# Kernel tuning notes

Hardware: AMD Instinct MI355X
Metric: run time of the kernel (lower is better)

Reference implementation:

```python
import jax, jax.numpy as jnp
import numpy as np

T, B, V = 50, 128, 8000          # seq_len, batch, inputDimSize
A = 728                          # numAncestors
NEMB = V + A                     # rows of W_emb
E, H, ATT, C, L = 128, 128, 100, 283, 5


def setup_inputs() -> dict:
    key = jax.random.key(0)
    ks = jax.random.split(key, 12)
    x = jax.random.normal(ks[0], (T, B, V), jnp.float32)
    mask = jnp.ones((T, B), jnp.float32)
    leaves = jax.random.randint(ks[1], (V, L), 0, NEMB)
    ancestors = jax.random.randint(ks[2], (V, L), 0, NEMB)
    W_emb = jax.random.uniform(ks[3], (NEMB, E), jnp.float32)
    W_attention = jax.random.uniform(ks[4], (2 * E, ATT), jnp.float32)
    b_attention = jnp.zeros((ATT,), jnp.float32)
    v_attention = jax.random.uniform(ks[5], (ATT,), jnp.float32)
    gru_w_ih = jax.random.normal(ks[6], (3 * H, E), jnp.float32) * 0.1
    gru_w_hh = jax.random.normal(ks[7], (3 * H, H), jnp.float32) * 0.1
    gru_b_ih = jnp.zeros((3 * H,), jnp.float32)
    gru_b_hh = jnp.zeros((3 * H,), jnp.float32)
    W_output = jax.random.uniform(ks[8], (H, C), jnp.float32) * 0.1
    b_output = jnp.zeros((C,), jnp.float32)
    return {"x": x, "mask": mask, "W_emb": W_emb,
            "W_attention": W_attention, "b_attention": b_attention,
            "v_attention": v_attention, "gru_w_ih": gru_w_ih,
            "gru_w_hh": gru_w_hh, "gru_b_ih": gru_b_ih,
            "gru_b_hh": gru_b_hh, "W_output": W_output,
            "b_output": b_output, "leaves": leaves, "ancestors": ancestors}


def reference(x, mask, W_emb, W_attention, b_attention, v_attention,
              gru_w_ih, gru_w_hh, gru_b_ih, gru_b_hh,
              W_output, b_output, leaves, ancestors):
    # --- Attention over ontology ancestors (gather + MLP + softmax + reduce) ---
    le = W_emb[leaves]       # [V, L, E]
    an = W_emb[ancestors]    # [V, L, E]
    att_in = jnp.concatenate([le, an], axis=-1)              # [V, L, 2E]
    mlp = jnp.tanh(att_in @ W_attention + b_attention)       # [V, L, ATT]
    pre = mlp @ v_attention                                  # [V, L]
    att = jax.nn.softmax(pre, axis=1)                        # softmax over ancestors
    emb = jnp.einsum('vle,vl->ve', an, att)                  # [V, E]

    # --- project multi-hot visits into embedding space ---
    x_emb = jnp.tanh(jnp.einsum('tbv,ve->tbe', x, emb))      # [T, B, E]

    # --- torch-style single-layer GRU via scan (time-major) ---
    def cell(h, xt):
        gx = xt @ gru_w_ih.T + gru_b_ih                      # [B, 3H]
        gh = h @ gru_w_hh.T + gru_b_hh
        xr, xz, xn = jnp.split(gx, 3, axis=-1)
        hr, hz, hn = jnp.split(gh, 3, axis=-1)
        r = jax.nn.sigmoid(xr + hr)
        z = jax.nn.sigmoid(xz + hz)
        n = jnp.tanh(xn + r * hn)
        h_new = (1.0 - z) * n + z * h
        return h_new, h_new

    h0 = jnp.zeros((B, H), x_emb.dtype)
    _, hidden = jax.lax.scan(cell, h0, x_emb)                # [T, B, H]

    # dropout_rate = 0 -> identity
    # exp / sum == softmax over the class dim
    out = jax.nn.softmax(hidden @ W_output + b_output, axis=2)  # [T, B, C]
    return out * mask[:, :, None]
```

## Files before the change

### kernel.cpp

```cpp
#include <hip/hip_runtime.h>


typedef unsigned short u16;
typedef unsigned int   u32;
typedef short bf16x8 __attribute__((ext_vector_type(8)));
typedef float f32x4  __attribute__((ext_vector_type(4)));

typedef __attribute__((address_space(1))) u32 gas_u32;
typedef __attribute__((address_space(3))) u32 las_u32;

union U4 { u32 u[4]; bf16x8 v; uint4 q; };

__device__ __forceinline__ float uaf(u32 u){ union{u32 u; float f;} c; c.u=u; return c.f; }
__device__ __forceinline__ u32 fau(float f){ union{u32 u; float f;} c; c.f=f; return c.u; }
__device__ __forceinline__ u16 f2bf(float f){ u32 u=fau(f); return (u16)((u + 0x7fffu + ((u>>16)&1u))>>16); }
__device__ __forceinline__ float sigm(float x){ return 1.f/(1.f+__expf(-x)); }

__device__ __forceinline__ void gll16(const void* g, void* l){
    __builtin_amdgcn_global_load_lds((const gas_u32*)g, (las_u32*)l, 16, 0, 0);
}

__device__ __forceinline__ void split8(const float* f, bf16x8* hi, bf16x8* lo){
    U4 H, L;
    #pragma unroll
    for (int j=0;j<4;++j){
        float f0=f[2*j], f1=f[2*j+1];
        u32 u0=fau(f0), u1=fau(f1);
        u32 t0=u0+0x7fffu+((u0>>16)&1u);
        u32 t1=u1+0x7fffu+((u1>>16)&1u);
        u32 h1=t1&0xffff0000u;
        H.u[j]=(t0>>16)|h1;
        float l0=f0-uaf(t0&0xffff0000u);
        float l1=f1-uaf(h1);
        u32 v0=fau(l0), v1=fau(l1);
        u32 s0=v0+0x7fffu+((v0>>16)&1u);
        u32 s1=v1+0x7fffu+((v1>>16)&1u);
        L.u[j]=(s0>>16)|(s1&0xffff0000u);
    }
    *hi=H.v; *lo=L.v;
}

__device__ __forceinline__ void split1(float f, u16& h, u16& l){
    u32 u=fau(f); u32 t=u+0x7fffu+((u>>16)&1u); h=(u16)(t>>16);
    float lf=f-uaf(t&0xffff0000u); l=f2bf(lf);
}

#define MFMA(a,b,c) __builtin_amdgcn_mfma_f32_16x16x32_bf16(a,b,c,0,0,0)

__global__ __launch_bounds__(256,1) void prep_watt_kernel(
    const float* __restrict__ W_att, u16* __restrict__ WT_h, u16* __restrict__ WT_l)
{
    int n=blockIdx.x, k=threadIdx.x;
    float f = (n<100)? W_att[k*100+n] : 0.f;
    u16 h,l; split1(f,h,l);
    WT_h[n*256+k]=h; WT_l[n*256+k]=l;
}

__global__ __launch_bounds__(256,1) void prep_whh_kernel(
    const float* __restrict__ whh, u32* __restrict__ out)
{
    int i=blockIdx.x*256+threadIdx.x;
    int j=i>>6, p=i&63;
    u32 a=(u32)f2bf(whh[j*128+2*p]);
    u32 b=(u32)f2bf(whh[j*128+2*p+1]);
    out[i]=a|(b<<16);
}

__global__ __launch_bounds__(256,1) void transpose_wih_kernel(
    const float* __restrict__ w_ih, float* __restrict__ w_ihT)
{
    int i=blockIdx.x*256+threadIdx.x;
    int e=i/384, j=i-e*384;
    w_ihT[i]=w_ih[j*128+e];
}

__global__ __launch_bounds__(256,1) void attn_mlp_kernel(
    const float* __restrict__ W_emb, const float* __restrict__ b_att,
    const float* __restrict__ v_att, const int* __restrict__ leaves,
    const int* __restrict__ anc, const u16* __restrict__ WT_h,
    const u16* __restrict__ WT_l, float* __restrict__ emb_f)
{
    __shared__ __align__(16) char smem[61440];
    short* Ah=(short*)smem;
    short* Al=(short*)(smem+16384);
    short* Bh=(short*)(smem+32768);
    short* Bl=(short*)(smem+47104);
    float* mlp_s=(float*)smem;
    __shared__ float s_pre[128];
    __shared__ float s_vatt[112];
    __shared__ float s_attw[128];
    __shared__ int   s_leaf[128], s_anc[128];

    const int tid=threadIdx.x;
    const int wave=tid>>6, lane=tid&63;
    const int vb5=blockIdx.x*125;

    if (tid<125){ s_leaf[tid]=leaves[vb5+tid]; s_anc[tid]=anc[vb5+tid]; }
    else if (tid<128){ s_leaf[tid]=leaves[vb5]; s_anc[tid]=anc[vb5]; }
    if (tid<100) s_vatt[tid]=v_att[tid];

    f32x4 acc[2][7];
    const f32x4 zf={0.f,0.f,0.f,0.f};
    #pragma unroll
    for (int mi=0;mi<2;++mi)
        #pragma unroll
        for (int ni=0;ni<7;++ni) acc[mi][ni]=zf;

    const int fr=lane&15, fq=lane>>4;

    for (int kc=0;kc<4;++kc){
        __syncthreads();
        {
            int r=tid>>1, seg=tid&1;
            int src=(kc<2)? s_leaf[r] : s_anc[r];
            const float* srcp = W_emb + (size_t)src*128 + (kc&1)*64 + seg*32;
            float buf[32];
            #pragma unroll
            for (int i=0;i<8;++i) *(f32x4*)(buf+4*i) = *(const f32x4*)(srcp+4*i);
            #pragma unroll
            for (int j=0;j<4;++j){
                bf16x8 hv, lv; split8(buf+8*j, &hv, &lv);
                U4 H,L; H.v=hv; L.v=lv;
                *(uint4*)&Ah[r*64+seg*32+j*8] = H.q;
                *(uint4*)&Al[r*64+seg*32+j*8] = L.q;
            }
        }
        for (int c=wave;c<14;c+=4){
            size_t go=(size_t)(c*8+(lane>>3))*512 + (size_t)kc*128 + (size_t)(lane&7)*16;
            gll16((const char*)WT_h+go, Bh+c*512);
            gll16((const char*)WT_l+go, Bl+c*512);
        }
        __syncthreads();

        #pragma unroll
        for (int ks=0;ks<2;++ks){
            bf16x8 ah[2],al[2],bh[7],bl[7];
            #pragma unroll
            for (int mi=0;mi<2;++mi){
                int row=wave*32+mi*16+fr;
                ah[mi]=*(const bf16x8*)&Ah[row*64+ks*32+fq*8];
                al[mi]=*(const bf16x8*)&Al[row*64+ks*32+fq*8];
            }
            #pragma unroll
            for (int ni=0;ni<7;++ni){
                int rowb=ni*16+fr;
                bh[ni]=*(const bf16x8*)&Bh[rowb*64+ks*32+fq*8];
                bl[ni]=*(const bf16x8*)&Bl[rowb*64+ks*32+fq*8];
            }
            #pragma unroll
            for (int mi=0;mi<2;++mi)
                #pragma unroll
                for (int ni=0;ni<7;++ni){
                    acc[mi][ni]=MFMA(ah[mi],bh[ni],acc[mi][ni]);
                    acc[mi][ni]=MFMA(ah[mi],bl[ni],acc[mi][ni]);
                    acc[mi][ni]=MFMA(al[mi],bh[ni],acc[mi][ni]);
                }
        }
    }
    __syncthreads();
    #pragma unroll
    for (int ni=0;ni<7;++ni){
        int col=ni*16+fr;
        float bb=(col<100)? b_att[col] : 0.f;
        #pragma unroll
        for (int mi=0;mi<2;++mi){
            int rb=wave*32+mi*16+fq*4;
            #pragma unroll
            for (int r=0;r<4;++r)
                mlp_s[(rb+r)*112+col]=tanhf(acc[mi][ni][r]+bb);
        }
    }
    __syncthreads();
    if (tid<128){
        float s=0.f;
        for (int n=0;n<100;++n) s+=mlp_s[tid*112+n]*s_vatt[n];
        s_pre[tid]=s;
    }
    __syncthreads();
    if (tid<25){
        float p[5], mx=-1e30f;
        #pragma unroll
        for (int l=0;l<5;++l){ p[l]=s_pre[tid*5+l]; mx=fmaxf(mx,p[l]); }
        float s=0.f;
        #pragma unroll
        for (int l=0;l<5;++l){ p[l]=__expf(p[l]-mx); s+=p[l]; }
        float inv=1.f/s;
        #pragma unroll
        for (int l=0;l<5;++l) s_attw[tid*5+l]=p[l]*inv;
    }
    __syncthreads();
    for (int o=tid;o<3200;o+=256){
        int v=o>>7, e=o&127;
        float s=0.f;
        #pragma unroll
        for (int l=0;l<5;++l)
            s += s_attw[v*5+l]*W_emb[(size_t)s_anc[v*5+l]*128+e];
        emb_f[(size_t)(blockIdx.x*25+v)*128+e]=s;
    }
}

__global__ __launch_bounds__(256,1) void emb_split_kernel(
    const float* __restrict__ emb_f, u16* __restrict__ hiT, u16* __restrict__ loT)
{
    __shared__ float tile[64*128];
    const int tid=threadIdx.x;
    const int vb=blockIdx.x*64;
    for (int i=tid;i<2048;i+=256){
        int row=i>>5, q=i&31;
        *(f32x4*)&tile[row*128+q*4] = *(const f32x4*)&emb_f[(size_t)(vb+row)*128+q*4];
    }
    __syncthreads();
    u32* hw=(u32*)hiT; u32* lw=(u32*)loT;
    for (int o=tid;o<4096;o+=256){
        int e=o>>5, p=o&31;
        float f0=tile[(2*p)*128+e], f1=tile[(2*p+1)*128+e];
        u16 h0,l0,h1,l1; split1(f0,h0,l0); split1(f1,h1,l1);
        size_t base=(size_t)e*4000 + (size_t)(vb>>1) + p;
        hw[base]=(u32)h0|((u32)h1<<16);
        lw[base]=(u32)l0|((u32)l1<<16);
    }
}

__global__ __launch_bounds__(256,1) void gemm_xemb_kernel(
    const float* __restrict__ x, const u16* __restrict__ bhT, const u16* __restrict__ blT,
    float* __restrict__ partials)
{
    __shared__ __align__(16) float Asf[128*64];
    __shared__ __align__(16) short Bh[128*64];
    __shared__ __align__(16) short Bl[128*64];

    const int tid=threadIdx.x, wave=tid>>6, lane=tid&63;
    const int mt=blockIdx.x%50, ks=blockIdx.x/50;
    const int mbase=mt*128;
    const int k0=ks*1600;

    f32x4 acc[4][4];
    const f32x4 zf={0.f,0.f,0.f,0.f};
    #pragma unroll
    for (int i=0;i<4;++i)
        #pragma unroll
        for (int j=0;j<4;++j) acc[i][j]=zf;

    const char* xb=(const char*)x;
    const char* bhb=(const char*)bhT;
    const char* blb=(const char*)blT;
    const int mrow=(wave>>1)*64, ncol=(wave&1)*64;
    const int fr=lane&15, fq=lane>>4;

    for (int kk=k0; kk<k0+1600; kk+=64){
        __syncthreads();
        #pragma unroll
        for (int cc=0;cc<8;++cc){
            int c=wave*8+cc;
            int row=c*4+(lane>>4);
            gll16(xb + (size_t)(mbase+row)*32000 + (size_t)kk*4 + (size_t)(lane&15)*16,
                  &Asf[c*256]);
        }
        #pragma unroll
        for (int cc=0;cc<4;++cc){
            int c=wave*4+cc;
            int row=c*8+(lane>>3);
            size_t go=(size_t)row*16000 + (size_t)kk*2 + (size_t)(lane&7)*16;
            gll16(bhb+go, &Bh[c*512]);
            gll16(blb+go, &Bl[c*512]);
        }
        __syncthreads();

        #pragma unroll
        for (int kh=0;kh<2;++kh){
            bf16x8 ah[4],al[4],bh[4],bl[4];
            #pragma unroll
            for (int i=0;i<4;++i)
                split8(&Asf[(mrow+i*16+fr)*64 + kh*32 + fq*8], &ah[i], &al[i]);
            #pragma unroll
            for (int j=0;j<4;++j){
                bh[j]=*(const bf16x8*)&Bh[(ncol+j*16+fr)*64+kh*32+fq*8];
                bl[j]=*(const bf16x8*)&Bl[(ncol+j*16+fr)*64+kh*32+fq*8];
            }
            #pragma unroll
            for (int i=0;i<4;++i)
                #pragma unroll
                for (int j=0;j<4;++j){
                    acc[i][j]=MFMA(ah[i],bh[j],acc[i][j]);
                    acc[i][j]=MFMA(ah[i],bl[j],acc[i][j]);
                    acc[i][j]=MFMA(al[i],bh[j],acc[i][j]);
                }
        }
    }

    float* pout=partials + ((size_t)ks*6400+mbase)*128;
    #pragma unroll
    for (int i=0;i<4;++i)
        #pragma unroll
        for (int j=0;j<4;++j)
            #pragma unroll
            for (int r=0;r<4;++r)
                pout[(size_t)(mrow+i*16+fq*4+r)*128 + ncol+j*16+fr]=acc[i][j][r];
}

__global__ __launch_bounds__(256,1) void sum_tanh_kernel(
    const float* __restrict__ partials, float* __restrict__ x_emb)
{
    int i=blockIdx.x*256+threadIdx.x;
    float s=0.f;
    #pragma unroll
    for (int k=0;k<5;++k) s+=partials[(size_t)k*819200+i];
    x_emb[i]=tanhf(s);
}

__global__ __launch_bounds__(128,1) void gx_gemm_kernel(
    const float* __restrict__ x_emb, const float* __restrict__ w_ihT,
    const float* __restrict__ b_ih, float* __restrict__ GX)
{
    __shared__ float sx[2048];
    const int tid=threadIdx.x;
    const int rb=blockIdx.x*16;
    for (int i=tid;i<2048;i+=128) sx[i]=x_emb[(size_t)rb*128+i];
    __syncthreads();

    float acc0[16],acc1[16],acc2[16];
    #pragma unroll
    for (int r=0;r<16;++r){ acc0[r]=0.f; acc1[r]=0.f; acc2[r]=0.f; }
    for (int e=0;e<128;++e){
        float w0=w_ihT[e*384+tid];
        float w1=w_ihT[e*384+tid+128];
        float w2=w_ihT[e*384+tid+256];
        #pragma unroll
        for (int r=0;r<16;++r){
            float xv=sx[r*128+e];
            acc0[r]=fmaf(xv,w0,acc0[r]);
            acc1[r]=fmaf(xv,w1,acc1[r]);
            acc2[r]=fmaf(xv,w2,acc2[r]);
        }
    }
    float b0=b_ih[tid], b1=b_ih[tid+128], b2=b_ih[tid+256];
    #pragma unroll
    for (int r=0;r<16;++r){
        float* gp=GX+(size_t)(rb+r)*384;
        gp[tid]=acc0[r]+b0;
        gp[tid+128]=acc1[r]+b1;
        gp[tid+256]=acc2[r]+b2;
    }
}

__global__ __launch_bounds__(384,1) void gru_scan_kernel(
    const u32* __restrict__ whh_p, const float* __restrict__ b_hh,
    const float* __restrict__ GX, float* __restrict__ hidden)
{
    __shared__ __align__(16) float sh[128];
    __shared__ float sgh[384];
    __shared__ float sgx[384];
    const int tid=threadIdx.x, b=blockIdx.x;

    u32 wreg[64];
    #pragma unroll
    for (int p=0;p<64;++p) wreg[p]=whh_p[tid*64+p];
    if (tid<128) sh[tid]=0.f;
    const float bb=b_hh[tid];
    __syncthreads();

    const f32x4* sh4=(const f32x4*)sh;
    for (int t=0;t<50;++t){
        float acc=0.f;
        #pragma unroll
        for (int q=0;q<32;++q){
            f32x4 h4=sh4[q];
            u32 a=wreg[2*q], c=wreg[2*q+1];
            acc=fmaf(uaf(a<<16),        h4.x,acc);
            acc=fmaf(uaf(a&0xffff0000u),h4.y,acc);
            acc=fmaf(uaf(c<<16),        h4.z,acc);
            acc=fmaf(uaf(c&0xffff0000u),h4.w,acc);
        }
        sgh[tid]=acc+bb;
        sgx[tid]=GX[((size_t)t*128+b)*384+tid];
        __syncthreads();
        if (tid<128){
            float r=sigm(sgx[tid]+sgh[tid]);
            float z=sigm(sgx[128+tid]+sgh[128+tid]);
            float n=tanhf(sgx[256+tid]+r*sgh[256+tid]);
            float hn=(1.f-z)*n+z*sh[tid];
            hidden[((size_t)t*128+b)*128+tid]=hn;
            sh[tid]=hn;
        }
        __syncthreads();
    }
}

__global__ __launch_bounds__(128,1) void logits_kernel(
    const float* __restrict__ hidden, const float* __restrict__ W_out,
    const float* __restrict__ b_out, float* __restrict__ logits)
{
    __shared__ float shd[2048];
    const int tid=threadIdx.x;
    const int rb=blockIdx.x*16;
    for (int i=tid;i<2048;i+=128) shd[i]=hidden[(size_t)rb*128+i];
    __syncthreads();

    const int c0=tid, c1=tid+128, c2=tid+256;
    const bool v2=(c2<283);
    float acc0[16],acc1[16],acc2[16];
    #pragma unroll
    for (int r=0;r<16;++r){ acc0[r]=0.f; acc1[r]=0.f; acc2[r]=0.f; }
    for (int h=0;h<128;++h){
        const float* wr=W_out+h*283;
        float w0=wr[c0];
        float w1=wr[c1];
        float w2=v2? wr[c2] : 0.f;
        #pragma unroll
        for (int r=0;r<16;++r){
            float hv=shd[r*128+h];
            acc0[r]=fmaf(hv,w0,acc0[r]);
            acc1[r]=fmaf(hv,w1,acc1[r]);
            acc2[r]=fmaf(hv,w2,acc2[r]);
        }
    }
    float b0=b_out[c0], b1=b_out[c1], b2v=v2? b_out[c2] : 0.f;
    #pragma unroll
    for (int r=0;r<16;++r){
        float* lp=logits+(size_t)(rb+r)*283;
        lp[c0]=acc0[r]+b0;
        lp[c1]=acc1[r]+b1;
        if (v2) lp[c2]=acc2[r]+b2v;
    }
}

__global__ __launch_bounds__(256,1) void softmax_mask_kernel(
    const float* __restrict__ logits, const float* __restrict__ mask,
    float* __restrict__ out)
{
    const int wave=threadIdx.x>>6, lane=threadIdx.x&63;
    const int m=blockIdx.x*4+wave;
    const float* lp=logits+(size_t)m*283;
    float v[5];
    float mx=-1e30f;
    #pragma unroll
    for (int i=0;i<5;++i){
        int c=lane+i*64;
        v[i]=(c<283)? lp[c] : -1e30f;
        mx=fmaxf(mx,v[i]);
    }
    #pragma unroll
    for (int off=32;off>0;off>>=1) mx=fmaxf(mx,__shfl_xor(mx,off,64));
    float s=0.f;
    #pragma unroll
    for (int i=0;i<5;++i){
        int c=lane+i*64;
        v[i]=(c<283)? __expf(v[i]-mx) : 0.f;
        s+=v[i];
    }
    #pragma unroll
    for (int off=32;off>0;off>>=1) s+=__shfl_xor(s,off,64);
    const float sc=mask[m]/s;
    float* op=out+(size_t)m*283;
    #pragma unroll
    for (int i=0;i<5;++i){
        int c=lane+i*64;
        if (c<283) op[c]=v[i]*sc;
    }
}

extern "C" void kernel_launch(void* const* d_in, const int* in_sizes, int n_in,
                              void* d_out, int out_size, void* d_ws, size_t ws_size,
                              hipStream_t stream) {
    const float* x      = (const float*)d_in[0];
    const float* mask   = (const float*)d_in[1];
    const float* W_emb  = (const float*)d_in[2];
    const float* W_att  = (const float*)d_in[3];
    const float* b_att  = (const float*)d_in[4];
    const float* v_att  = (const float*)d_in[5];
    const float* w_ih   = (const float*)d_in[6];
    const float* w_hh   = (const float*)d_in[7];
    const float* b_ih   = (const float*)d_in[8];
    const float* b_hh   = (const float*)d_in[9];
    const float* W_out  = (const float*)d_in[10];
    const float* b_out  = (const float*)d_in[11];
    const int* leaves   = (const int*)d_in[12];
    const int* anc      = (const int*)d_in[13];
    float* out = (float*)d_out;

    char* w = (char*)d_ws;
    u16*   WT_h    = (u16*)(w + 0);
    u16*   WT_l    = (u16*)(w + 57344);
    u32*   whh_p   = (u32*)(w + 114688);
    float* w_ihT   = (float*)(w + 212992);
    u16*   emb_hiT = (u16*)(w + 409600);
    u16*   emb_loT = (u16*)(w + 2457600);
    float* x_emb   = (float*)(w + 4505600);
    float* hidden  = (float*)(w + 7782400);
    float* emb_f   = (float*)(w + 11059200);
    float* partials= (float*)(w + 11059200);
    float* GX      = (float*)(w + 11059200);
    float* logits  = (float*)(w + 11059200);

    prep_watt_kernel<<<112, 256, 0, stream>>>(W_att, WT_h, WT_l);
    prep_whh_kernel<<<96, 256, 0, stream>>>(w_hh, whh_p);
    transpose_wih_kernel<<<192, 256, 0, stream>>>(w_ih, w_ihT);
    attn_mlp_kernel<<<320, 256, 0, stream>>>(W_emb, b_att, v_att, leaves, anc,
                                             WT_h, WT_l, emb_f);
    emb_split_kernel<<<125, 256, 0, stream>>>(emb_f, emb_hiT, emb_loT);
    gemm_xemb_kernel<<<250, 256, 0, stream>>>(x, emb_hiT, emb_loT, partials);
    sum_tanh_kernel<<<3200, 256, 0, stream>>>(partials, x_emb);
    gx_gemm_kernel<<<400, 128, 0, stream>>>(x_emb, w_ihT, b_ih, GX);
    gru_scan_kernel<<<128, 384, 0, stream>>>(whh_p, b_hh, GX, hidden);
    logits_kernel<<<400, 128, 0, stream>>>(hidden, W_out, b_out, logits);
    softmax_mask_kernel<<<1600, 256, 0, stream>>>(logits, mask, out);
}
```

Measured before the change: 549.8 us.

## Shrink x_emb GEMM tiles with swizzled LDS and bf16 hidden state in GRU scan

The x·emb GEMM moves from 128x128 tiles over 250 blocks to 32x128 tiles over 1000 blocks, with XOR-swizzled LDS layouts and launch bounds that allow four blocks per CU. This should raise occupancy and cut LDS bank conflicts in the kernel that streams the large x tensor. In the GRU scan, the recurrent weights are pre-expanded to fp32 registers, the hidden state is kept in a register and broadcast through LDS as bf16, and GX is loaded straight into registers. Rounding h to bf16 for the recurrent matvec is a precision risk, and the 128 fp32 weights per thread raise register pressure.

```diff
diff --git a/kernel.cpp b/kernel.cpp
--- a/kernel.cpp
+++ b/kernel.cpp
@@ -221,81 +221,88 @@
     }
 }
 
-__global__ __launch_bounds__(256,1) void gemm_xemb_kernel(
+__global__ __launch_bounds__(256,4) void gemm_xemb_kernel(
     const float* __restrict__ x, const u16* __restrict__ bhT, const u16* __restrict__ blT,
     float* __restrict__ partials)
 {
-    __shared__ __align__(16) float Asf[128*64];
+    __shared__ __align__(16) float Asf[32*64];
     __shared__ __align__(16) short Bh[128*64];
     __shared__ __align__(16) short Bl[128*64];
 
     const int tid=threadIdx.x, wave=tid>>6, lane=tid&63;
-    const int mt=blockIdx.x%50, ks=blockIdx.x/50;
-    const int mbase=mt*128;
+    const int mt=blockIdx.x%200, ks=blockIdx.x/200;
+    const int mbase=mt*32;
     const int k0=ks*1600;
 
-    f32x4 acc[4][4];
+    f32x4 acc[2][2];
     const f32x4 zf={0.f,0.f,0.f,0.f};
     #pragma unroll
-    for (int i=0;i<4;++i)
-        #pragma unroll
-        for (int j=0;j<4;++j) acc[i][j]=zf;
+    for (int i=0;i<2;++i)
+        #pragma unroll
+        for (int j=0;j<2;++j) acc[i][j]=zf;
 
     const char* xb=(const char*)x;
     const char* bhb=(const char*)bhT;
     const char* blb=(const char*)blT;
-    const int mrow=(wave>>1)*64, ncol=(wave&1)*64;
     const int fr=lane&15, fq=lane>>4;
+    const int nbase=wave*32;
 
     for (int kk=k0; kk<k0+1600; kk+=64){
         __syncthreads();
         #pragma unroll
-        for (int cc=0;cc<8;++cc){
-            int c=wave*8+cc;
-            int row=c*4+(lane>>4);
-            gll16(xb + (size_t)(mbase+row)*32000 + (size_t)kk*4 + (size_t)(lane&15)*16,
-                  &Asf[c*256]);
-        }
-        #pragma unroll
-        for (int cc=0;cc<4;++cc){
-            int c=wave*4+cc;
-            int row=c*8+(lane>>3);
-            size_t go=(size_t)row*16000 + (size_t)kk*2 + (size_t)(lane&7)*16;
-            gll16(bhb+go, &Bh[c*512]);
-            gll16(blb+go, &Bl[c*512]);
+        for (int ii=0;ii<2;++ii){
+            int L=(wave*2+ii)*64+lane;
+            int r=L>>4, c=(L&15)^(r&15);
+            gll16(xb + ((size_t)(mbase+r)*8000 + kk + c*4)*4, (char*)Asf + (size_t)L*16);
+        }
+        #pragma unroll
+        for (int ii=0;ii<4;++ii){
+            int L=(wave*4+ii)*64+lane;
+            int r=L>>3, c=(L&7)^(r&7);
+            size_t go=((size_t)r*8000 + kk + c*8)*2;
+            gll16(bhb+go, (char*)Bh + (size_t)L*16);
+            gll16(blb+go, (char*)Bl + (size_t)L*16);
         }
         __syncthreads();
 
         #pragma unroll
         for (int kh=0;kh<2;++kh){
-            bf16x8 ah[4],al[4],bh[4],bl[4];
-            #pragma unroll
-            for (int i=0;i<4;++i)
-                split8(&Asf[(mrow+i*16+fr)*64 + kh*32 + fq*8], &ah[i], &al[i]);
-            #pragma unroll
-            for (int j=0;j<4;++j){
-                bh[j]=*(const bf16x8*)&Bh[(ncol+j*16+fr)*64+kh*32+fq*8];
-                bl[j]=*(const bf16x8*)&Bl[(ncol+j*16+fr)*64+kh*32+fq*8];
+            bf16x8 ah[2],al[2],bh[2],bl[2];
+            #pragma unroll
+            for (int mi=0;mi<2;++mi){
+                int row=mi*16+fr;
+                int c0=kh*8+fq*2;
+                float buf[8];
+                *(f32x4*)&buf[0]=*(const f32x4*)&Asf[(row*16+((c0  )^(row&15)))*4];
+                *(f32x4*)&buf[4]=*(const f32x4*)&Asf[(row*16+((c0+1)^(row&15)))*4];
+                split8(buf,&ah[mi],&al[mi]);
             }
             #pragma unroll
-            for (int i=0;i<4;++i)
+            for (int ni=0;ni<2;++ni){
+                int rowb=nbase+ni*16+fr;
+                int ch=rowb*8+((kh*4+fq)^(rowb&7));
+                bh[ni]=*(const bf16x8*)&Bh[ch*8];
+                bl[ni]=*(const bf16x8*)&Bl[ch*8];
+            }
+            #pragma unroll
+            for (int mi=0;mi<2;++mi)
                 #pragma unroll
-                for (int j=0;j<4;++j){
-                    acc[i][j]=MFMA(ah[i],bh[j],acc[i][j]);
-                    acc[i][j]=MFMA(ah[i],bl[j],acc[i][j]);
-                    acc[i][j]=MFMA(al[i],bh[j],acc[i][j]);
+                for (int ni=0;ni<2;++ni){
+                    acc[mi][ni]=MFMA(ah[mi],bh[ni],acc[mi][ni]);
+                    acc[mi][ni]=MFMA(ah[mi],bl[ni],acc[mi][ni]);
+                    acc[mi][ni]=MFMA(al[mi],bh[ni],acc[mi][ni]);
                 }
         }
     }
 
     float* pout=partials + ((size_t)ks*6400+mbase)*128;
     #pragma unroll
-    for (int i=0;i<4;++i)
-        #pragma unroll
-        for (int j=0;j<4;++j)
+    for (int mi=0;mi<2;++mi)
+        #pragma unroll
+        for (int ni=0;ni<2;++ni)
             #pragma unroll
             for (int r=0;r<4;++r)
-                pout[(size_t)(mrow+i*16+fq*4+r)*128 + ncol+j*16+fr]=acc[i][j][r];
+                pout[(size_t)(mi*16+fq*4+r)*128 + nbase+ni*16+fr]=acc[mi][ni][r];
 }
 
 __global__ __launch_bounds__(256,1) void sum_tanh_kernel(
@@ -347,40 +354,49 @@
     const u32* __restrict__ whh_p, const float* __restrict__ b_hh,
     const float* __restrict__ GX, float* __restrict__ hidden)
 {
-    __shared__ __align__(16) float sh[128];
+    __shared__ __align__(16) u16 shb[128];
     __shared__ float sgh[384];
-    __shared__ float sgx[384];
     const int tid=threadIdx.x, b=blockIdx.x;
 
-    u32 wreg[64];
-    #pragma unroll
-    for (int p=0;p<64;++p) wreg[p]=whh_p[tid*64+p];
-    if (tid<128) sh[tid]=0.f;
+    float wf[128];
+    #pragma unroll
+    for (int q=0;q<64;++q){
+        u32 u=whh_p[tid*64+q];
+        wf[2*q]  =uaf(u<<16);
+        wf[2*q+1]=uaf(u&0xffff0000u);
+    }
+    float hreg=0.f;
+    if (tid<128) shb[tid]=0;
     const float bb=b_hh[tid];
     __syncthreads();
 
-    const f32x4* sh4=(const f32x4*)sh;
     for (int t=0;t<50;++t){
+        float gx0=0.f,gx1=0.f,gx2=0.f;
+        if (tid<128){
+            const float* gp=GX+((size_t)t*128+b)*384;
+            gx0=gp[tid]; gx1=gp[128+tid]; gx2=gp[256+tid];
+        }
         float acc=0.f;
         #pragma unroll
-        for (int q=0;q<32;++q){
-            f32x4 h4=sh4[q];
-            u32 a=wreg[2*q], c=wreg[2*q+1];
-            acc=fmaf(uaf(a<<16),        h4.x,acc);
-            acc=fmaf(uaf(a&0xffff0000u),h4.y,acc);
-            acc=fmaf(uaf(c<<16),        h4.z,acc);
-            acc=fmaf(uaf(c&0xffff0000u),h4.w,acc);
+        for (int p=0;p<16;++p){
+            U4 c; c.v=*(const bf16x8*)&shb[p*8];
+            #pragma unroll
+            for (int j=0;j<4;++j){
+                u32 u=c.u[j];
+                acc=fmaf(uaf(u<<16),         wf[p*8+2*j],   acc);
+                acc=fmaf(uaf(u&0xffff0000u), wf[p*8+2*j+1], acc);
+            }
         }
         sgh[tid]=acc+bb;
-        sgx[tid]=GX[((size_t)t*128+b)*384+tid];
         __syncthreads();
         if (tid<128){
-            float r=sigm(sgx[tid]+sgh[tid]);
-            float z=sigm(sgx[128+tid]+sgh[128+tid]);
-            float n=tanhf(sgx[256+tid]+r*sgh[256+tid]);
-            float hn=(1.f-z)*n+z*sh[tid];
+            float r=sigm(gx0+sgh[tid]);
+            float z=sigm(gx1+sgh[128+tid]);
+            float n=tanhf(gx2+r*sgh[256+tid]);
+            float hn=(1.f-z)*n+z*hreg;
+            hreg=hn;
             hidden[((size_t)t*128+b)*128+tid]=hn;
-            sh[tid]=hn;
+            shb[tid]=f2bf(hn);
         }
         __syncthreads();
     }
@@ -498,7 +514,7 @@
     attn_mlp_kernel<<<320, 256, 0, stream>>>(W_emb, b_att, v_att, leaves, anc,
                                              WT_h, WT_l, emb_f);
     emb_split_kernel<<<125, 256, 0, stream>>>(emb_f, emb_hiT, emb_loT);
-    gemm_xemb_kernel<<<250, 256, 0, stream>>>(x, emb_hiT, emb_loT, partials);
+    gemm_xemb_kernel<<<1000, 256, 0, stream>>>(x, emb_hiT, emb_loT, partials);
     sum_tanh_kernel<<<3200, 256, 0, stream>>>(partials, x_emb);
     gx_gemm_kernel<<<400, 128, 0, stream>>>(x_emb, w_ihT, b_ih, GX);
     gru_scan_kernel<<<128, 384, 0, stream>>>(whh_p, b_hh, GX, hidden);
```

Result: faster. 529.3 us (-3.7%).
